# Optimization experiments

Hardware: AMD Instinct MI355X
Metric: run time of the kernel (lower is better)

The kernel has to match this reference:

```python
import jax, jax.numpy as jnp
import numpy as np

DIM = 512
HEADS = 8
DIM_HEAD = 64
INNER = HEADS * DIM_HEAD  # 512
SCALE = DIM_HEAD ** -0.5
LN_EPS = 1e-5


def setup_inputs() -> dict:
    key = jax.random.key(0)
    k1, k2, k3, k4 = jax.random.split(key, 4)
    b, p, n = 4, 64, 256
    x = jax.random.normal(k1, (b, p, n, DIM), dtype=jnp.float32)
    ln_g = jnp.ones((DIM,), jnp.float32)
    ln_b = jnp.zeros((DIM,), jnp.float32)
    # stored as [in, out] for x @ W
    w_qkv = jax.random.normal(k2, (DIM, 3 * INNER), jnp.float32) * (DIM ** -0.5)
    w_out = jax.random.normal(k3, (INNER, DIM), jnp.float32) * (INNER ** -0.5)
    b_out = jnp.zeros((DIM,), jnp.float32)
    return {"x": x, "ln_g": ln_g, "ln_b": ln_b, "w_qkv": w_qkv,
            "w_out": w_out, "b_out": b_out}


def reference(x, ln_g, ln_b, w_qkv, w_out, b_out):
    b, p, n, _ = x.shape
    # LayerNorm over last dim
    mu = jnp.mean(x, axis=-1, keepdims=True)
    var = jnp.mean(jnp.square(x - mu), axis=-1, keepdims=True)
    xn = (x - mu) * jax.lax.rsqrt(var + LN_EPS) * ln_g + ln_b
    # QKV projection (no bias)
    qkv = xn @ w_qkv                                   # [b,p,n,3*INNER]
    q, k, v = jnp.split(qkv, 3, axis=-1)
    def to_heads(t):
        return t.reshape(b, p, n, HEADS, DIM_HEAD).transpose(0, 1, 3, 2, 4)
    q, k, v = to_heads(q), to_heads(k), to_heads(v)    # [b,p,h,n,d]
    dots = jnp.einsum('bphnd,bphmd->bphnm', q, k) * SCALE
    attn = jax.nn.softmax(dots, axis=-1)
    out = jnp.einsum('bphnm,bphmd->bphnd', attn, v)    # [b,p,h,n,d]
    out = out.transpose(0, 1, 3, 2, 4).reshape(b, p, n, INNER)
    return out @ w_out + b_out
```

## Files before the change

### kernel.cpp

```cpp
#include <hip/hip_runtime.h>
#include <stdint.h>

#define DIMD 512
#define HEADS 8
#define DHEAD 64
#define NSEQ 256
#define NGRP 256
#define TRIPLE 1536
#define ATT_SCALE 0.125f

typedef float f32x4 __attribute__((ext_vector_type(4)));
typedef _Float16 half8 __attribute__((ext_vector_type(8)));
typedef _Float16 half4 __attribute__((ext_vector_type(4)));

#define GLD16(gp, lp) __builtin_amdgcn_global_load_lds( \
    (const __attribute__((address_space(1))) void*)(gp), \
    (__attribute__((address_space(3))) void*)(lp), 16, 0, 0)
#define BAR() __builtin_amdgcn_s_barrier()
#define VMW(n) asm volatile("s_waitcnt vmcnt(" #n ")" ::: "memory")
#define LGKM0() asm volatile("s_waitcnt lgkmcnt(0)" ::: "memory")

__global__ __launch_bounds__(256) void k_pre(const float* __restrict__ x,
                                             const float* __restrict__ g,
                                             const float* __restrict__ b,
                                             const float* __restrict__ wq,
                                             const float* __restrict__ wo,
                                             _Float16* __restrict__ xn,
                                             _Float16* __restrict__ wtq,
                                             _Float16* __restrict__ wto) {
  int bid = blockIdx.x;
  if (bid < 256) {
    __shared__ float T[64][65];
    const float* src; _Float16* dst; int spitch, ti, tj;
    if (bid < 192) { src = wq; dst = wtq; spitch = TRIPLE; ti = bid / 24; tj = bid % 24; }
    else { int t = bid - 192; src = wo; dst = wto; spitch = DIMD; ti = t >> 3; tj = t & 7; }
#pragma unroll
    for (int it = 0; it < 4; ++it) {
      int idx = it * 256 + threadIdx.x;
      int rr = idx >> 4, c4 = (idx & 15) * 4;
      *(f32x4*)&T[rr][c4] = *(const f32x4*)&src[(size_t)(ti * 64 + rr) * spitch + tj * 64 + c4];
    }
    __syncthreads();
#pragma unroll
    for (int it = 0; it < 2; ++it) {
      int idx = it * 256 + threadIdx.x;
      int rr2 = idx >> 3, c8 = (idx & 7) * 8;
      half8 o;
#pragma unroll
      for (int j = 0; j < 8; ++j) o[j] = (_Float16)T[c8 + j][rr2];
      *(half8*)&dst[(size_t)(tj * 64 + rr2) * DIMD + ti * 64 + c8] = o;
    }
    return;
  }
  int row = (bid - 256) * 4 + (threadIdx.x >> 6);
  int lane = threadIdx.x & 63;
  const float* xr = x + (size_t)row * DIMD + lane * 8;
  float v[8];
  *(f32x4*)(v)     = *(const f32x4*)(xr);
  *(f32x4*)(v + 4) = *(const f32x4*)(xr + 4);
  float s = 0.f, ss = 0.f;
#pragma unroll
  for (int j = 0; j < 8; ++j) { s += v[j]; ss += v[j] * v[j]; }
#pragma unroll
  for (int m = 1; m < 64; m <<= 1) { s += __shfl_xor(s, m); ss += __shfl_xor(ss, m); }
  float mean = s * (1.f / DIMD);
  float var  = ss * (1.f / DIMD) - mean * mean;
  float rstd = rsqrtf(var + 1e-5f);
  const float* gp = g + lane * 8;
  const float* bp = b + lane * 8;
  half8 o;
#pragma unroll
  for (int j = 0; j < 8; ++j) o[j] = (_Float16)((v[j] - mean) * rstd * gp[j] + bp[j]);
  *(half8*)(xn + (size_t)row * DIMD + lane * 8) = o;
}

template <int N, int LDA, bool F32OUT>
__global__ __launch_bounds__(512, 2) void k_gemm8(const _Float16* __restrict__ A,
                                                  const _Float16* __restrict__ BT,
                                                  _Float16* __restrict__ Ch,
                                                  float* __restrict__ Cf,
                                                  const float* __restrict__ bias) {
  constexpr int NT = N / 256;
  constexpr int NWG = 256 * NT;
  constexpr int CPX = NWG / 8;
  int bb_ = blockIdx.x;
  int logical = (bb_ & 7) * CPX + (bb_ >> 3);
  int mt = logical / NT, nt = logical % NT;
  int m0 = mt * 256, n0 = nt * 256;

  int tid = threadIdx.x, lane = tid & 63, w = tid >> 6;
  int wrow = w >> 2, wcol = w & 3;
  int l15 = lane & 15, lg = lane >> 4;
  const int sr = lane >> 3;
  const int ss = lane & 7;

  __shared__ _Float16 S[65536];

  f32x4 acc[8][4] = {};
  half8 af0[4][2], af1[4][2], bf0[2][2], bf1[2][2];

  auto stageA = [&](int d, int kt, int hf) {
#pragma unroll
    for (int cc = 0; cc < 2; ++cc) {
      int rbase = cc * 128 + hf * 64 + w * 8;
      const _Float16* gp = A + (size_t)(m0 + rbase + sr) * LDA + kt * 64 + (ss ^ sr) * 8;
      GLD16(gp, &S[d * 32768 + rbase * 64]);
    }
  };
  auto stageB = [&](int d, int kt, int hf) {
#pragma unroll
    for (int cc = 0; cc < 2; ++cc) {
      int i = cc * 64 + w * 8;
      int rbase = (i >> 5) * 64 + hf * 32 + (i & 31);
      const _Float16* gp = BT + (size_t)(n0 + rbase + sr) * 512 + kt * 64 + (ss ^ sr) * 8;
      GLD16(gp, &S[d * 32768 + 16384 + rbase * 64]);
    }
  };
  auto loadA = [&](int c, int mh, half8 (&af)[4][2]) {
#pragma unroll
    for (int mf = 0; mf < 4; ++mf) {
      int row = wrow * 128 + mh * 64 + mf * 16 + l15;
#pragma unroll
      for (int kk = 0; kk < 2; ++kk) {
        int byte = row * 128 + ((kk * 64 + lg * 16) ^ ((row & 7) << 4));
        af[mf][kk] = *(const half8*)((const char*)&S[c * 32768] + byte);
      }
    }
  };
  auto loadB = [&](int c, int nh, half8 (&bf)[2][2]) {
#pragma unroll
    for (int nf = 0; nf < 2; ++nf) {
      int row = wcol * 64 + nh * 32 + nf * 16 + l15;
#pragma unroll
      for (int kk = 0; kk < 2; ++kk) {
        int byte = row * 128 + ((kk * 64 + lg * 16) ^ ((row & 7) << 4));
        bf[nf][kk] = *(const half8*)((const char*)&S[c * 32768 + 16384] + byte);
      }
    }
  };
  auto quad = [&](int mh, int nh, half8 (&af)[4][2], half8 (&bf)[2][2]) {
    __builtin_amdgcn_s_setprio(1);
#pragma unroll
    for (int mf = 0; mf < 4; ++mf)
#pragma unroll
      for (int nf = 0; nf < 2; ++nf)
#pragma unroll
        for (int kk = 0; kk < 2; ++kk)
          acc[mh * 4 + mf][nh * 2 + nf] = __builtin_amdgcn_mfma_f32_16x16x32_f16(
              af[mf][kk], bf[nf][kk], acc[mh * 4 + mf][nh * 2 + nf], 0, 0, 0);
    __builtin_amdgcn_s_setprio(0);
  };

  stageA(0, 0, 0); stageB(0, 0, 0); stageB(0, 0, 1); stageA(0, 0, 1);
  VMW(4); BAR();

#pragma unroll
  for (int t = 0; t < 8; ++t) {
    const int c = t & 1, d = c ^ 1;
    loadA(c, 0, af0); loadB(c, 0, bf0);
    if (t > 0) quad(1, 1, af1, bf1);
    if (t < 7) { stageA(d, t + 1, 0); VMW(4); } else { VMW(2); }
    BAR();
    loadB(c, 1, bf1);
    quad(0, 0, af0, bf0);
    if (t < 7) { stageB(d, t + 1, 0); VMW(4); } else { VMW(0); }
    BAR();
    loadA(c, 1, af1);
    quad(0, 1, af0, bf1);
    if (t < 7) stageB(d, t + 1, 1);
    BAR();
    quad(1, 0, af1, bf0);
    if (t < 7) { stageA(d, t + 1, 1); VMW(4); }
    BAR();
  }
  quad(1, 1, af1, bf1);

  char* Sb = (char*)S;
  if constexpr (!F32OUT) {
    __syncthreads();
#pragma unroll
    for (int mq = 0; mq < 8; ++mq)
#pragma unroll
      for (int nq = 0; nq < 4; ++nq)
#pragma unroll
        for (int r = 0; r < 4; ++r) {
          int row = wrow * 128 + (mq >> 2) * 64 + (mq & 3) * 16 + lg * 4 + r;
          int col = wcol * 64 + (nq >> 1) * 32 + (nq & 1) * 16 + l15;
          *(_Float16*)(Sb + row * 512 + ((col * 2) ^ ((row & 7) << 4))) =
              (_Float16)acc[mq][nq][r];
        }
    __syncthreads();
#pragma unroll
    for (int it = 0; it < 16; ++it) {
      int idx = it * 512 + tid;
      int row = idx >> 5, ch = idx & 31;
      half8 vv = *(const half8*)(Sb + row * 512 + ((ch * 16) ^ ((row & 7) << 4)));
      *(half8*)&Ch[(size_t)(m0 + row) * N + n0 + ch * 8] = vv;
    }
  } else {
    float bbv[4];
#pragma unroll
    for (int nq = 0; nq < 4; ++nq)
      bbv[nq] = bias[n0 + wcol * 64 + (nq >> 1) * 32 + (nq & 1) * 16 + l15];
    __syncthreads();
#pragma unroll
    for (int hh = 0; hh < 2; ++hh) {
      if (hh) { LGKM0(); BAR(); }
#pragma unroll
      for (int m2 = 0; m2 < 4; ++m2)
#pragma unroll
        for (int nq = 0; nq < 4; ++nq)
#pragma unroll
          for (int r = 0; r < 4; ++r) {
            int packed = wrow * 64 + m2 * 16 + lg * 4 + r;
            int col = wcol * 64 + (nq >> 1) * 32 + (nq & 1) * 16 + l15;
            *(float*)(Sb + packed * 1024 + ((col * 4) ^ ((packed & 7) << 4))) =
                acc[hh * 4 + m2][nq][r] + bbv[nq];
          }
      LGKM0(); BAR();
#pragma unroll
      for (int it = 0; it < 16; ++it) {
        int idx = it * 512 + tid;
        int prow = idx >> 6, ch = idx & 63;
        f32x4 vv = *(const f32x4*)(Sb + prow * 1024 + ((ch * 16) ^ ((prow & 7) << 4)));
        int row = (prow >> 6) * 128 + hh * 64 + (prow & 63);
        *(f32x4*)&Cf[(size_t)(m0 + row) * N + n0 + ch * 4] = vv;
      }
    }
  }
}

__global__ __launch_bounds__(256, 2) void k_attn(_Float16* __restrict__ qkv) {
  int g = blockIdx.x >> 3, h = blockIdx.x & 7;
  int tid = threadIdx.x, lane = tid & 63, w = tid >> 6;
  int l15 = lane & 15, lg = lane >> 4;
  __shared__ _Float16 Kt[2][64 * 64];
  __shared__ _Float16 Vt[2][64 * 72];
  __shared__ _Float16 Pl[4][64 * 72];
  const size_t base = (size_t)g * NSEQ * TRIPLE;
  const int srow = lane >> 3, sslot = lane & 7;

  half8 vr[2];
  auto vload = [&](int kt) {
#pragma unroll
    for (int i = 0; i < 2; ++i) {
      int idx = tid + i * 256;
      int key = idx >> 3, dh0 = (idx & 7) * 8;
      vr[i] = *(const half8*)&qkv[base + (size_t)(kt * 64 + key) * TRIPLE + 1024 + h * 64 + dh0];
    }
  };
  auto kstage = [&](int dbuf, int kt) {
#pragma unroll
    for (int rnd = 0; rnd < 2; ++rnd) {
      int rbase = rnd * 32 + w * 8;
      const _Float16* gp = &qkv[base + (size_t)(kt * 64 + rbase + srow) * TRIPLE
                                + 512 + h * 64 + (sslot ^ srow) * 8];
      GLD16(gp, &Kt[dbuf][rbase * 64]);
    }
  };
  auto vwrite = [&](int dbuf) {
#pragma unroll
    for (int i = 0; i < 2; ++i) {
      int idx = tid + i * 256;
      int key = idx >> 3, dh0 = (idx & 7) * 8;
#pragma unroll
      for (int j = 0; j < 8; ++j) Vt[dbuf][(dh0 + j) * 72 + key] = vr[i][j];
    }
  };

  half8 qf[4][2];
#pragma unroll
  for (int nq = 0; nq < 4; ++nq)
#pragma unroll
    for (int kd = 0; kd < 2; ++kd)
      qf[nq][kd] = *(const half8*)&qkv[base + (size_t)(w * 64 + nq * 16 + l15) * TRIPLE
                                       + h * 64 + kd * 32 + lg * 8];

  f32x4 oacc[4][4] = {};
  float mrun[4], lrun[4];
#pragma unroll
  for (int nq = 0; nq < 4; ++nq) { mrun[nq] = -3.0e38f; lrun[nq] = 0.f; }

  kstage(0, 0); vload(0);
  VMW(0);
  vwrite(0);
  LGKM0(); BAR();

  for (int kt = 0; kt < 4; ++kt) {
    const int c = kt & 1, d = c ^ 1;
    if (kt < 3) { kstage(d, kt + 1); vload(kt + 1); }

    f32x4 st[4][4] = {};
#pragma unroll
    for (int kd = 0; kd < 2; ++kd) {
      half8 kf[4];
#pragma unroll
      for (int mk = 0; mk < 4; ++mk) {
        int r = mk * 16 + l15;
        int byte = r * 128 + ((kd * 64 + lg * 16) ^ ((r & 7) << 4));
        kf[mk] = *(const half8*)((const char*)Kt[c] + byte);
      }
#pragma unroll
      for (int mk = 0; mk < 4; ++mk)
#pragma unroll
        for (int nq = 0; nq < 4; ++nq)
          st[mk][nq] = __builtin_amdgcn_mfma_f32_16x16x32_f16(kf[mk], qf[nq][kd], st[mk][nq], 0, 0, 0);
    }

    float alpha[4];
#pragma unroll
    for (int nq = 0; nq < 4; ++nq) {
      float pm = -3.0e38f;
#pragma unroll
      for (int mk = 0; mk < 4; ++mk)
#pragma unroll
        for (int r = 0; r < 4; ++r) {
          st[mk][nq][r] *= ATT_SCALE;
          pm = fmaxf(pm, st[mk][nq][r]);
        }
      pm = fmaxf(pm, __shfl_xor(pm, 16));
      pm = fmaxf(pm, __shfl_xor(pm, 32));
      float mn = fmaxf(mrun[nq], pm);
      alpha[nq] = __expf(mrun[nq] - mn);
      mrun[nq] = mn;
      float ps = 0.f;
#pragma unroll
      for (int mk = 0; mk < 4; ++mk) {
        half4 p4;
#pragma unroll
        for (int r = 0; r < 4; ++r) {
          float e = __expf(st[mk][nq][r] - mn);
          ps += e;
          p4[r] = (_Float16)e;
        }
        *(half4*)&Pl[w][(nq * 16 + l15) * 72 + mk * 16 + lg * 4] = p4;
      }
      ps += __shfl_xor(ps, 16);
      ps += __shfl_xor(ps, 32);
      lrun[nq] = lrun[nq] * alpha[nq] + ps;
    }

#pragma unroll
    for (int mp = 0; mp < 4; ++mp)
#pragma unroll
      for (int r = 0; r < 4; ++r) {
        float av = __shfl(alpha[mp], lg * 4 + r);
#pragma unroll
        for (int nd = 0; nd < 4; ++nd) oacc[mp][nd][r] *= av;
      }

    LGKM0();
    __builtin_amdgcn_sched_barrier(0);

#pragma unroll
    for (int kp = 0; kp < 2; ++kp) {
      int co = kp * 32 + lg * 8;
      half8 pf[4], vf[4];
#pragma unroll
      for (int mp = 0; mp < 4; ++mp) pf[mp] = *(const half8*)&Pl[w][(mp * 16 + l15) * 72 + co];
#pragma unroll
      for (int nd = 0; nd < 4; ++nd) vf[nd] = *(const half8*)&Vt[c][(nd * 16 + l15) * 72 + co];
#pragma unroll
      for (int mp = 0; mp < 4; ++mp)
#pragma unroll
        for (int nd = 0; nd < 4; ++nd)
          oacc[mp][nd] = __builtin_amdgcn_mfma_f32_16x16x32_f16(pf[mp], vf[nd], oacc[mp][nd], 0, 0, 0);
    }

    if (kt < 3) { VMW(0); vwrite(d); }
    LGKM0(); BAR();
  }

#pragma unroll
  for (int mp = 0; mp < 4; ++mp)
#pragma unroll
    for (int r = 0; r < 4; ++r) {
      float li = 1.f / __shfl(lrun[mp], lg * 4 + r);
      int q = w * 64 + mp * 16 + lg * 4 + r;
#pragma unroll
      for (int nd = 0; nd < 4; ++nd)
        qkv[base + (size_t)q * TRIPLE + h * 64 + nd * 16 + l15] =
            (_Float16)(oacc[mp][nd][r] * li);
    }
}

extern "C" void kernel_launch(void* const* d_in, const int* in_sizes, int n_in,
                              void* d_out, int out_size, void* d_ws, size_t ws_size,
                              hipStream_t stream) {
  const float* x     = (const float*)d_in[0];
  const float* ln_g  = (const float*)d_in[1];
  const float* ln_b  = (const float*)d_in[2];
  const float* w_qkv = (const float*)d_in[3];
  const float* w_out = (const float*)d_in[4];
  const float* b_out = (const float*)d_in[5];

  char* ws = (char*)d_ws;
  _Float16* qkv = (_Float16*)ws;
  _Float16* wtq = (_Float16*)(ws + 201326592ull);
  _Float16* wto = (_Float16*)(ws + 201326592ull + 1572864ull);
  _Float16* xn  = (_Float16*)d_out;
  float* out    = (float*)d_out;

  k_pre<<<16640, 256, 0, stream>>>(x, ln_g, ln_b, w_qkv, w_out, xn, wtq, wto);
  k_gemm8<TRIPLE, DIMD, false><<<1536, 512, 0, stream>>>(xn, wtq, qkv, nullptr, nullptr);
  k_attn<<<2048, 256, 0, stream>>>(qkv);
  k_gemm8<DIMD, TRIPLE, true><<<512, 512, 0, stream>>>(qkv, wto, nullptr, out, b_out);
}
```

Measured before the change: 281.1 us.

## Fuse QKV projection GEMM with attention per group-head in one kernel

Repacks the QKV weights per head so a single block computes the Q, K and V slices (256x192) for one group and head, keeps them in LDS, and runs the softmax attention directly from shared memory. This removes the fp16 qkv round-trip through HBM and one kernel launch, and the output GEMM now reads a compact 512-wide attention buffer. In exchange, each block has 8 waves with only 32 queries each, LDS use is large, and xn is re-read by 8 head blocks. It also adds a V-transpose scatter into LDS. The unused gemm path's F32OUT=false epilogue was simplified to direct stores.

```diff
diff --git a/kernel.cpp b/kernel.cpp
--- a/kernel.cpp
+++ b/kernel.cpp
@@ -5,7 +5,6 @@
 #define HEADS 8
 #define DHEAD 64
 #define NSEQ 256
-#define NGRP 256
 #define TRIPLE 1536
 #define ATT_SCALE 0.125f
 
@@ -26,14 +25,14 @@
                                              const float* __restrict__ wq,
                                              const float* __restrict__ wo,
                                              _Float16* __restrict__ xn,
-                                             _Float16* __restrict__ wtq,
+                                             _Float16* __restrict__ wth,
                                              _Float16* __restrict__ wto) {
   int bid = blockIdx.x;
   if (bid < 256) {
     __shared__ float T[64][65];
-    const float* src; _Float16* dst; int spitch, ti, tj;
-    if (bid < 192) { src = wq; dst = wtq; spitch = TRIPLE; ti = bid / 24; tj = bid % 24; }
-    else { int t = bid - 192; src = wo; dst = wto; spitch = DIMD; ti = t >> 3; tj = t & 7; }
+    const float* src; _Float16* dst; int spitch, ti, tj; bool packed;
+    if (bid < 192) { src = wq; dst = wth; spitch = TRIPLE; ti = bid / 24; tj = bid % 24; packed = true; }
+    else { int t = bid - 192; src = wo; dst = wto; spitch = DIMD; ti = t >> 3; tj = t & 7; packed = false; }
 #pragma unroll
     for (int it = 0; it < 4; ++it) {
       int idx = it * 256 + threadIdx.x;
@@ -48,7 +47,8 @@
       half8 o;
 #pragma unroll
       for (int j = 0; j < 8; ++j) o[j] = (_Float16)T[c8 + j][rr2];
-      *(half8*)&dst[(size_t)(tj * 64 + rr2) * DIMD + ti * 64 + c8] = o;
+      int drow = packed ? ((tj & 7) * 192 + (tj >> 3) * 64 + rr2) : (tj * 64 + rr2);
+      *(half8*)&dst[(size_t)drow * DIMD + ti * 64 + c8] = o;
     }
     return;
   }
@@ -72,6 +72,226 @@
 #pragma unroll
   for (int j = 0; j < 8; ++j) o[j] = (_Float16)((v[j] - mean) * rstd * gp[j] + bp[j]);
   *(half8*)(xn + (size_t)row * DIMD + lane * 8) = o;
+}
+
+__global__ __launch_bounds__(512, 2) void k_fused(const _Float16* __restrict__ A,
+                                                  const _Float16* __restrict__ BT,
+                                                  _Float16* __restrict__ att) {
+  int bphys = blockIdx.x;
+  int logical = (bphys & 7) * 256 + (bphys >> 3);
+  int g = logical >> 3, h = logical & 7;
+  int m0 = g * 256;
+
+  int tid = threadIdx.x, lane = tid & 63, w = tid >> 6;
+  int wrow = w >> 2, wcol = w & 3;
+  int l15 = lane & 15, lg = lane >> 4;
+  const int sr = lane >> 3, ss = lane & 7;
+
+  __shared__ _Float16 LB[57344];
+
+  f32x4 acc[8][3] = {};
+  half8 af0[4][2], af1[4][2], bfE[3][2], bfO[3][2];
+
+  auto stageA = [&](int d, int kt, int hf) {
+#pragma unroll
+    for (int cc = 0; cc < 2; ++cc) {
+      int rbase = cc * 128 + hf * 64 + w * 8;
+      const _Float16* gp = A + (size_t)(m0 + rbase + sr) * 512 + kt * 64 + (ss ^ sr) * 8;
+      GLD16(gp, &LB[d * 28672 + rbase * 64]);
+    }
+  };
+  auto stageB = [&](int d, int kt) {
+#pragma unroll
+    for (int cc = 0; cc < 3; ++cc) {
+      int rbase = w * 24 + cc * 8;
+      const _Float16* gp = BT + (size_t)(h * 192 + rbase + sr) * 512 + kt * 64 + (ss ^ sr) * 8;
+      GLD16(gp, &LB[d * 28672 + 16384 + rbase * 64]);
+    }
+  };
+  auto loadA = [&](int c, int mh, half8 (&af)[4][2]) {
+#pragma unroll
+    for (int mf = 0; mf < 4; ++mf) {
+      int row = wrow * 128 + mh * 64 + mf * 16 + l15;
+#pragma unroll
+      for (int kk = 0; kk < 2; ++kk) {
+        int byte = row * 128 + ((kk * 64 + lg * 16) ^ ((row & 7) << 4));
+        af[mf][kk] = *(const half8*)((const char*)&LB[c * 28672] + byte);
+      }
+    }
+  };
+  auto loadB = [&](int c, half8 (&bf)[3][2]) {
+#pragma unroll
+    for (int nf = 0; nf < 3; ++nf) {
+      int row = wcol * 48 + nf * 16 + l15;
+#pragma unroll
+      for (int kk = 0; kk < 2; ++kk) {
+        int byte = row * 128 + ((kk * 64 + lg * 16) ^ ((row & 7) << 4));
+        bf[nf][kk] = *(const half8*)((const char*)&LB[c * 28672 + 16384] + byte);
+      }
+    }
+  };
+  auto quad = [&](int mh, half8 (&af)[4][2], half8 (&bf)[3][2]) {
+    __builtin_amdgcn_s_setprio(1);
+#pragma unroll
+    for (int mf = 0; mf < 4; ++mf)
+#pragma unroll
+      for (int nf = 0; nf < 3; ++nf)
+#pragma unroll
+        for (int kk = 0; kk < 2; ++kk)
+          acc[mh * 4 + mf][nf] = __builtin_amdgcn_mfma_f32_16x16x32_f16(
+              af[mf][kk], bf[nf][kk], acc[mh * 4 + mf][nf], 0, 0, 0);
+    __builtin_amdgcn_s_setprio(0);
+  };
+
+  stageA(0, 0, 0); stageB(0, 0); stageA(0, 0, 1);
+  VMW(2); BAR();
+
+#pragma unroll
+  for (int t = 0; t < 8; ++t) {
+    const int c = t & 1, d = c ^ 1;
+    const bool even = (t & 1) == 0;
+    loadA(c, 0, af0);
+    if (even) loadB(c, bfE); else loadB(c, bfO);
+    if (t > 0) { if (even) quad(1, af1, bfO); else quad(1, af1, bfE); }
+    if (t < 7) { stageA(d, t + 1, 0); stageB(d, t + 1); VMW(5); }
+    else VMW(0);
+    BAR();
+    loadA(c, 1, af1);
+    if (even) quad(0, af0, bfE); else quad(0, af0, bfO);
+    if (t < 7) { stageA(d, t + 1, 1); VMW(2); }
+    BAR();
+  }
+  quad(1, af1, bfO);
+
+  _Float16* Ks = LB;
+  _Float16* Vt = LB + 16384;
+  _Float16* Qs = LB + 33280;
+  _Float16* Pw = LB + 33280 + w * 2304;
+
+#pragma unroll
+  for (int mq = 0; mq < 8; ++mq)
+#pragma unroll
+    for (int nf = 0; nf < 3; ++nf)
+#pragma unroll
+      for (int r = 0; r < 4; ++r) {
+        int row = wrow * 128 + (mq >> 2) * 64 + (mq & 3) * 16 + lg * 4 + r;
+        int col = wcol * 48 + nf * 16 + l15;
+        _Float16 v = (_Float16)acc[mq][nf][r];
+        int third = col >> 6, dh = col & 63;
+        if (third == 0)
+          *(_Float16*)((char*)Qs + row * 128 + ((dh * 2) ^ ((row & 7) << 4))) = v;
+        else if (third == 1)
+          *(_Float16*)((char*)Ks + row * 128 + ((dh * 2) ^ ((row & 7) << 4))) = v;
+        else
+          Vt[dh * 264 + row] = v;
+      }
+  __syncthreads();
+
+  half8 qf[2][2];
+#pragma unroll
+  for (int nq = 0; nq < 2; ++nq)
+#pragma unroll
+    for (int kd = 0; kd < 2; ++kd) {
+      int qrow = w * 32 + nq * 16 + l15;
+      qf[nq][kd] = *(const half8*)((const char*)Qs + qrow * 128 +
+                                   ((kd * 64 + lg * 16) ^ ((qrow & 7) << 4)));
+    }
+  __syncthreads();
+
+  f32x4 oacc[2][4] = {};
+  float mrun[2] = {-3.0e38f, -3.0e38f}, lrun[2] = {0.f, 0.f};
+
+  for (int kt = 0; kt < 4; ++kt) {
+    f32x4 st[4][2] = {};
+#pragma unroll
+    for (int kd = 0; kd < 2; ++kd) {
+      half8 kf[4];
+#pragma unroll
+      for (int mk = 0; mk < 4; ++mk) {
+        int krow = kt * 64 + mk * 16 + l15;
+        kf[mk] = *(const half8*)((const char*)Ks + krow * 128 +
+                                 ((kd * 64 + lg * 16) ^ ((krow & 7) << 4)));
+      }
+#pragma unroll
+      for (int mk = 0; mk < 4; ++mk)
+#pragma unroll
+        for (int nq = 0; nq < 2; ++nq)
+          st[mk][nq] = __builtin_amdgcn_mfma_f32_16x16x32_f16(kf[mk], qf[nq][kd], st[mk][nq], 0, 0, 0);
+    }
+
+    float alpha[2];
+#pragma unroll
+    for (int nq = 0; nq < 2; ++nq) {
+      float pm = -3.0e38f;
+#pragma unroll
+      for (int mk = 0; mk < 4; ++mk)
+#pragma unroll
+        for (int r = 0; r < 4; ++r) {
+          st[mk][nq][r] *= ATT_SCALE;
+          pm = fmaxf(pm, st[mk][nq][r]);
+        }
+      pm = fmaxf(pm, __shfl_xor(pm, 16));
+      pm = fmaxf(pm, __shfl_xor(pm, 32));
+      float mn = fmaxf(mrun[nq], pm);
+      alpha[nq] = __expf(mrun[nq] - mn);
+      mrun[nq] = mn;
+      float ps = 0.f;
+#pragma unroll
+      for (int mk = 0; mk < 4; ++mk) {
+        half4 p4;
+#pragma unroll
+        for (int r = 0; r < 4; ++r) {
+          float e = __expf(st[mk][nq][r] - mn);
+          ps += e;
+          p4[r] = (_Float16)e;
+        }
+        *(half4*)&Pw[(nq * 16 + l15) * 72 + mk * 16 + lg * 4] = p4;
+      }
+      ps += __shfl_xor(ps, 16);
+      ps += __shfl_xor(ps, 32);
+      lrun[nq] = lrun[nq] * alpha[nq] + ps;
+    }
+
+#pragma unroll
+    for (int mp = 0; mp < 2; ++mp)
+#pragma unroll
+      for (int r = 0; r < 4; ++r) {
+        float av = __shfl(alpha[mp], lg * 4 + r);
+#pragma unroll
+        for (int nd = 0; nd < 4; ++nd) oacc[mp][nd][r] *= av;
+      }
+
+    LGKM0();
+    __builtin_amdgcn_sched_barrier(0);
+
+#pragma unroll
+    for (int kp = 0; kp < 2; ++kp) {
+      int co = kp * 32 + lg * 8;
+      half8 pf[2], vf[4];
+#pragma unroll
+      for (int mp = 0; mp < 2; ++mp) pf[mp] = *(const half8*)&Pw[(mp * 16 + l15) * 72 + co];
+#pragma unroll
+      for (int nd = 0; nd < 4; ++nd)
+        vf[nd] = *(const half8*)&Vt[(nd * 16 + l15) * 264 + kt * 64 + co];
+#pragma unroll
+      for (int mp = 0; mp < 2; ++mp)
+#pragma unroll
+        for (int nd = 0; nd < 4; ++nd)
+          oacc[mp][nd] = __builtin_amdgcn_mfma_f32_16x16x32_f16(pf[mp], vf[nd], oacc[mp][nd], 0, 0, 0);
+    }
+  }
+
+#pragma unroll
+  for (int mp = 0; mp < 2; ++mp)
+#pragma unroll
+    for (int r = 0; r < 4; ++r) {
+      float li = 1.f / __shfl(lrun[mp], lg * 4 + r);
+      int q = w * 32 + mp * 16 + lg * 4 + r;
+#pragma unroll
+      for (int nd = 0; nd < 4; ++nd)
+        att[(size_t)(g * 256 + q) * DIMD + h * 64 + nd * 16 + l15] =
+            (_Float16)(oacc[mp][nd][r] * li);
+    }
 }
 
 template <int N, int LDA, bool F32OUT>
@@ -184,19 +404,10 @@
       for (int nq = 0; nq < 4; ++nq)
 #pragma unroll
         for (int r = 0; r < 4; ++r) {
-          int row = wrow * 128 + (mq >> 2) * 64 + (mq & 3) * 16 + lg * 4 + r;
-          int col = wcol * 64 + (nq >> 1) * 32 + (nq & 1) * 16 + l15;
-          *(_Float16*)(Sb + row * 512 + ((col * 2) ^ ((row & 7) << 4))) =
-              (_Float16)acc[mq][nq][r];
+          int row = m0 + wrow * 128 + (mq >> 2) * 64 + (mq & 3) * 16 + lg * 4 + r;
+          int col = n0 + wcol * 64 + (nq >> 1) * 32 + (nq & 1) * 16 + l15;
+          Ch[(size_t)row * N + col] = (_Float16)acc[mq][nq][r];
         }
-    __syncthreads();
-#pragma unroll
-    for (int it = 0; it < 16; ++it) {
-      int idx = it * 512 + tid;
-      int row = idx >> 5, ch = idx & 31;
-      half8 vv = *(const half8*)(Sb + row * 512 + ((ch * 16) ^ ((row & 7) << 4)));
-      *(half8*)&Ch[(size_t)(m0 + row) * N + n0 + ch * 8] = vv;
-    }
   } else {
     float bbv[4];
 #pragma unroll
@@ -228,160 +439,6 @@
       }
     }
   }
-}
-
-__global__ __launch_bounds__(256, 2) void k_attn(_Float16* __restrict__ qkv) {
-  int g = blockIdx.x >> 3, h = blockIdx.x & 7;
-  int tid = threadIdx.x, lane = tid & 63, w = tid >> 6;
-  int l15 = lane & 15, lg = lane >> 4;
-  __shared__ _Float16 Kt[2][64 * 64];
-  __shared__ _Float16 Vt[2][64 * 72];
-  __shared__ _Float16 Pl[4][64 * 72];
-  const size_t base = (size_t)g * NSEQ * TRIPLE;
-  const int srow = lane >> 3, sslot = lane & 7;
-
-  half8 vr[2];
-  auto vload = [&](int kt) {
-#pragma unroll
-    for (int i = 0; i < 2; ++i) {
-      int idx = tid + i * 256;
-      int key = idx >> 3, dh0 = (idx & 7) * 8;
-      vr[i] = *(const half8*)&qkv[base + (size_t)(kt * 64 + key) * TRIPLE + 1024 + h * 64 + dh0];
-    }
-  };
-  auto kstage = [&](int dbuf, int kt) {
-#pragma unroll
-    for (int rnd = 0; rnd < 2; ++rnd) {
-      int rbase = rnd * 32 + w * 8;
-      const _Float16* gp = &qkv[base + (size_t)(kt * 64 + rbase + srow) * TRIPLE
-                                + 512 + h * 64 + (sslot ^ srow) * 8];
-      GLD16(gp, &Kt[dbuf][rbase * 64]);
-    }
-  };
-  auto vwrite = [&](int dbuf) {
-#pragma unroll
-    for (int i = 0; i < 2; ++i) {
-      int idx = tid + i * 256;
-      int key = idx >> 3, dh0 = (idx & 7) * 8;
-#pragma unroll
-      for (int j = 0; j < 8; ++j) Vt[dbuf][(dh0 + j) * 72 + key] = vr[i][j];
-    }
-  };
-
-  half8 qf[4][2];
-#pragma unroll
-  for (int nq = 0; nq < 4; ++nq)
-#pragma unroll
-    for (int kd = 0; kd < 2; ++kd)
-      qf[nq][kd] = *(const half8*)&qkv[base + (size_t)(w * 64 + nq * 16 + l15) * TRIPLE
-                                       + h * 64 + kd * 32 + lg * 8];
-
-  f32x4 oacc[4][4] = {};
-  float mrun[4], lrun[4];
-#pragma unroll
-  for (int nq = 0; nq < 4; ++nq) { mrun[nq] = -3.0e38f; lrun[nq] = 0.f; }
-
-  kstage(0, 0); vload(0);
-  VMW(0);
-  vwrite(0);
-  LGKM0(); BAR();
-
-  for (int kt = 0; kt < 4; ++kt) {
-    const int c = kt & 1, d = c ^ 1;
-    if (kt < 3) { kstage(d, kt + 1); vload(kt + 1); }
-
-    f32x4 st[4][4] = {};
-#pragma unroll
-    for (int kd = 0; kd < 2; ++kd) {
-      half8 kf[4];
-#pragma unroll
-      for (int mk = 0; mk < 4; ++mk) {
-        int r = mk * 16 + l15;
-        int byte = r * 128 + ((kd * 64 + lg * 16) ^ ((r & 7) << 4));
-        kf[mk] = *(const half8*)((const char*)Kt[c] + byte);
-      }
-#pragma unroll
-      for (int mk = 0; mk < 4; ++mk)
-#pragma unroll
-        for (int nq = 0; nq < 4; ++nq)
-          st[mk][nq] = __builtin_amdgcn_mfma_f32_16x16x32_f16(kf[mk], qf[nq][kd], st[mk][nq], 0, 0, 0);
-    }
-
-    float alpha[4];
-#pragma unroll
-    for (int nq = 0; nq < 4; ++nq) {
-      float pm = -3.0e38f;
-#pragma unroll
-      for (int mk = 0; mk < 4; ++mk)
-#pragma unroll
-        for (int r = 0; r < 4; ++r) {
-          st[mk][nq][r] *= ATT_SCALE;
-          pm = fmaxf(pm, st[mk][nq][r]);
-        }
-      pm = fmaxf(pm, __shfl_xor(pm, 16));
-      pm = fmaxf(pm, __shfl_xor(pm, 32));
-      float mn = fmaxf(mrun[nq], pm);
-      alpha[nq] = __expf(mrun[nq] - mn);
-      mrun[nq] = mn;
-      float ps = 0.f;
-#pragma unroll
-      for (int mk = 0; mk < 4; ++mk) {
-        half4 p4;
-#pragma unroll
-        for (int r = 0; r < 4; ++r) {
-          float e = __expf(st[mk][nq][r] - mn);
-          ps += e;
-          p4[r] = (_Float16)e;
-        }
-        *(half4*)&Pl[w][(nq * 16 + l15) * 72 + mk * 16 + lg * 4] = p4;
-      }
-      ps += __shfl_xor(ps, 16);
-      ps += __shfl_xor(ps, 32);
-      lrun[nq] = lrun[nq] * alpha[nq] + ps;
-    }
-
-#pragma unroll
-    for (int mp = 0; mp < 4; ++mp)
-#pragma unroll
-      for (int r = 0; r < 4; ++r) {
-        float av = __shfl(alpha[mp], lg * 4 + r);
-#pragma unroll
-        for (int nd = 0; nd < 4; ++nd) oacc[mp][nd][r] *= av;
-      }
-
-    LGKM0();
-    __builtin_amdgcn_sched_barrier(0);
-
-#pragma unroll
-    for (int kp = 0; kp < 2; ++kp) {
-      int co = kp * 32 + lg * 8;
-      half8 pf[4], vf[4];
-#pragma unroll
-      for (int mp = 0; mp < 4; ++mp) pf[mp] = *(const half8*)&Pl[w][(mp * 16 + l15) * 72 + co];
-#pragma unroll
-      for (int nd = 0; nd < 4; ++nd) vf[nd] = *(const half8*)&Vt[c][(nd * 16 + l15) * 72 + co];
-#pragma unroll
-      for (int mp = 0; mp < 4; ++mp)
-#pragma unroll
-        for (int nd = 0; nd < 4; ++nd)
-          oacc[mp][nd] = __builtin_amdgcn_mfma_f32_16x16x32_f16(pf[mp], vf[nd], oacc[mp][nd], 0, 0, 0);
-    }
-
-    if (kt < 3) { VMW(0); vwrite(d); }
-    LGKM0(); BAR();
-  }
-
-#pragma unroll
-  for (int mp = 0; mp < 4; ++mp)
-#pragma unroll
-    for (int r = 0; r < 4; ++r) {
-      float li = 1.f / __shfl(lrun[mp], lg * 4 + r);
-      int q = w * 64 + mp * 16 + lg * 4 + r;
-#pragma unroll
-      for (int nd = 0; nd < 4; ++nd)
-        qkv[base + (size_t)q * TRIPLE + h * 64 + nd * 16 + l15] =
-            (_Float16)(oacc[mp][nd][r] * li);
-    }
 }
 
 extern "C" void kernel_launch(void* const* d_in, const int* in_sizes, int n_in,
@@ -395,14 +452,13 @@
   const float* b_out = (const float*)d_in[5];
 
   char* ws = (char*)d_ws;
-  _Float16* qkv = (_Float16*)ws;
-  _Float16* wtq = (_Float16*)(ws + 201326592ull);
-  _Float16* wto = (_Float16*)(ws + 201326592ull + 1572864ull);
+  _Float16* att = (_Float16*)ws;
+  _Float16* wth = (_Float16*)(ws + 67108864ull);
+  _Float16* wto = (_Float16*)(ws + 67108864ull + 1572864ull);
   _Float16* xn  = (_Float16*)d_out;
   float* out    = (float*)d_out;
 
-  k_pre<<<16640, 256, 0, stream>>>(x, ln_g, ln_b, w_qkv, w_out, xn, wtq, wto);
-  k_gemm8<TRIPLE, DIMD, false><<<1536, 512, 0, stream>>>(xn, wtq, qkv, nullptr, nullptr);
-  k_attn<<<2048, 256, 0, stream>>>(qkv);
-  k_gemm8<DIMD, TRIPLE, true><<<512, 512, 0, stream>>>(qkv, wto, nullptr, out, b_out);
+  k_pre<<<16640, 256, 0, stream>>>(x, ln_g, ln_b, w_qkv, w_out, xn, wth, wto);
+  k_fused<<<2048, 512, 0, stream>>>(xn, wth, att);
+  k_gemm8<DIMD, DIMD, true><<<512, 512, 0, stream>>>(att, wto, nullptr, out, b_out);
 }
```

Result: no change. 281.6 us (+0.2%).
